# Optimization experiments

Measured on AMD Instinct MI355X. Metric: run time of the kernel, lower is better.

## Reference

```python
import jax, jax.numpy as jnp
import numpy as np

IMG = 160      # img_size
P = 100        # img_pathch_num = (160/16)^2
NBLK = 256     # pixels per 16x16 patch
NCLS = 4

def _index_matrix():
    # faithful port of NewAIFV.index_init
    ind = np.arange(256)
    start = (ind // 16) * IMG + (ind % 16) * 16
    idx = np.zeros(NBLK * P, dtype=np.int32)
    for i in range(P):
        idx[i * 256:(i + 1) * 256] = start + (i // 16) * 16 * IMG + (i % 16)
    return jnp.asarray(idx)

_IDX = _index_matrix()


def setup_inputs() -> dict:
    key = jax.random.key(0)
    ks = jax.random.split(key, 7)
    B, C = 4, 256
    return {
        "feat_S": jax.random.normal(ks[0], (B, C, IMG, IMG), jnp.float32),
        "feat_T": jax.random.normal(ks[1], (B, C, IMG, IMG), jnp.float32),
        "Pred_S": jax.random.normal(ks[2], (B, NCLS, IMG, IMG), jnp.float32),
        "Pred_T": jax.random.normal(ks[3], (B, NCLS, IMG, IMG), jnp.float32),
        "S_atten": jax.random.normal(ks[4], (B, P, P), jnp.float32),
        "T_atten": jax.random.normal(ks[5], (B, P, P), jnp.float32),
        "target": jax.random.randint(ks[6], (B, 1, IMG, IMG), 0, NCLS, jnp.int32),
    }


def _cos(a, b):
    # torch.nn.CosineSimilarity(dim=1): dot / max(|a||b|, 1e-8)
    num = (a * b).sum(1)
    den = jnp.maximum(jnp.sqrt((a * a).sum(1)) * jnp.sqrt((b * b).sum(1)), 1e-8)
    return num / den


def reference(feat_S, feat_T, Pred_S, Pred_T, S_atten, T_atten, target):
    B, C, H, W = feat_S.shape
    hw = H * W
    idx = _IDX
    # gathered patch reorder (index_select along flattened spatial dim)
    fS = feat_S.reshape(B, C, hw)[:, :, idx]
    fT = feat_T.reshape(B, C, hw)[:, :, idx]
    tg = target.reshape(B, 1, hw)[:, :, idx].reshape(B, 1, H, W)
    # 256-iteration loop of per-patch [B,C,100]@[B,100,100] matmuls -> one einsum
    TS = jnp.einsum('bcik,bkj->bcij', fS.reshape(B, C, NBLK, P), S_atten).reshape(B, C, H, W)
    TT = jnp.einsum('bcik,bkj->bcij', fT.reshape(B, C, NBLK, P), T_atten).reshape(B, C, H, W)
    ScS = jax.nn.softmax(Pred_S, axis=1).reshape(B, NCLS, hw)[:, :, idx].reshape(B, NCLS, H, W)
    ScT = jax.nn.softmax(Pred_T, axis=1).reshape(B, NCLS, hw)[:, :, idx].reshape(B, NCLS, H, W)
    dt = TS.dtype
    one_hot = (tg == jnp.arange(NCLS)[None, :, None, None]).astype(dt)   # [B,4,H,W]
    wei_s = (ScS * one_hot).sum(1)  # [B,H,W]
    wei_t = (ScT * one_hot).sum(1)
    tf = tg.astype(dt)  # [B,1,H,W], broadcast replaces nn.Upsample+expand

    def centers(class_list, s_prto, t_prto, eps):
        cS, cT = TS, TT
        for i in range(NCLS):
            j = class_list[i]
            stmp = ScT[:, j:j + 1]              # [B,1,H,W] (Score_Tmp, broadcast over C)
            m = (tf == i).astype(dt)            # mask_feat (class i)
            mp = (tf == j).astype(dt)           # mask_feat_prto (class class_list[i])
            denS = (mp if s_prto else m).sum((-1, -2)) + eps          # [B,1]
            protoS = ((mp * TS).sum((-1, -2)) / denS)[:, :, None, None]
            denT = (stmp * (mp if t_prto else m)).sum((-1, -2)) + eps
            protoT = ((mp * TT * stmp).sum((-1, -2)) / denT)[:, :, None, None]
            cS = (1 - m) * cS + m * protoS
            cT = (1 - m) * cT + m * protoT
        return cS, cT

    # three variants exactly as in the torch loops (denominator choices differ)
    cS0, cT0 = centers([1, 0, 3, 2], False, False, 1e-6)
    cS1, cT1 = centers([2, 3, 0, 1], True, True, 1e-6)
    cS2, cT2 = centers([3, 2, 1, 0], True, True, 1.0)

    w = (1 - wei_s) * wei_t
    vec_s = jnp.stack([w * _cos(TS, c) for c in (cS0, cS1, cS2)], axis=1)  # [B,3,H,W]
    vec_t = jnp.stack([w * _cos(TT, c) for c in (cT0, cT1, cT2)], axis=1)
    return jnp.mean((vec_s - vec_t) ** 2)
```

## Files before the change

kernel.cpp:

```cpp
#include <hip/hip_runtime.h>
#include <cstdint>
#include <cstddef>

#define HW 25600

typedef __attribute__((ext_vector_type(8))) short bf16x8;
typedef __attribute__((ext_vector_type(16))) float f32x16;

union ABu { bf16x8 v; uint2 u[2]; };
union B128 { bf16x8 v; int4 q; };

__device__ __forceinline__ f32x16 zero16() {
    f32x16 z;
#pragma unroll
    for (int i = 0; i < 16; ++i) z[i] = 0.f;
    return z;
}

__device__ __forceinline__ unsigned short f2bf(float x) {
    unsigned u = __builtin_bit_cast(unsigned, x);
    unsigned r = (u + 0x7FFF + ((u >> 16) & 1)) >> 16;
    return (unsigned short)r;
}

__device__ __forceinline__ float bf2f(unsigned short s) {
    return __builtin_bit_cast(float, (unsigned)s << 16);
}

__device__ __forceinline__ float wred(float v) {
#pragma unroll
    for (int off = 32; off; off >>= 1) v += __shfl_down(v, off, 64);
    return v;
}

__device__ double blockReduce256D(double v, double* s4) {
#pragma unroll
    for (int off = 32; off; off >>= 1) v += __shfl_down(v, off, 64);
    __syncthreads();
    if ((threadIdx.x & 63) == 0) s4[threadIdx.x >> 6] = v;
    __syncthreads();
    return s4[0] + s4[1] + s4[2] + s4[3];
}

__global__ __launch_bounds__(256) void k1_prep(
    const float* __restrict__ PredS, const float* __restrict__ PredT,
    const int* __restrict__ target,
    int* __restrict__ cls_arr, float* __restrict__ wT_arr,
    float* __restrict__ w_arr, float* __restrict__ partial_prep)
{
    __shared__ float sL[4][20];
    int blk = blockIdx.x;
    int b = blk / 100, r = blk - b * 100;
    int t = threadIdx.x, w = t >> 6, lane = t & 63;
    int ql = r * 256 + t;
    int v = ((t >> 4) * 160) + ((t & 15) * 16) + ((r >> 4) * 2560) + (r & 15);

    int cls = target[b * HW + v];

    const float* pS = PredS + b * 4 * HW + v;
    float a0 = pS[0], a1 = pS[HW], a2 = pS[2 * HW], a3 = pS[3 * HW];
    float mS = fmaxf(fmaxf(a0, a1), fmaxf(a2, a3));
    float e0 = expf(a0 - mS), e1 = expf(a1 - mS), e2 = expf(a2 - mS), e3 = expf(a3 - mS);
    float invS = 1.0f / (e0 + e1 + e2 + e3);
    float wei_s = ((cls == 0) ? e0 : (cls == 1) ? e1 : (cls == 2) ? e2 : e3) * invS;

    const float* pT = PredT + b * 4 * HW + v;
    float c0 = pT[0], c1 = pT[HW], c2 = pT[2 * HW], c3 = pT[3 * HW];
    float mT = fmaxf(fmaxf(c0, c1), fmaxf(c2, c3));
    float f0 = expf(c0 - mT), f1 = expf(c1 - mT), f2 = expf(c2 - mT), f3 = expf(c3 - mT);
    float invT = 1.0f / (f0 + f1 + f2 + f3);
    float tn0 = f0 * invT, tn1 = f1 * invT, tn2 = f2 * invT, tn3 = f3 * invT;
    float wei_t = (cls == 0) ? tn0 : (cls == 1) ? tn1 : (cls == 2) ? tn2 : tn3;

    cls_arr[b * HW + ql] = cls;
    wT_arr[b * HW + ql] = wei_t;
    w_arr[b * HW + ql] = (1.0f - wei_s) * wei_t;

    float vals[20];
#pragma unroll
    for (int s = 0; s < 4; ++s) vals[s] = (cls == s) ? 1.f : 0.f;
#pragma unroll
    for (int i2 = 0; i2 < 4; ++i2) {
        vals[4 + i2 * 4 + 0] = (cls == i2) ? tn0 : 0.f;
        vals[4 + i2 * 4 + 1] = (cls == i2) ? tn1 : 0.f;
        vals[4 + i2 * 4 + 2] = (cls == i2) ? tn2 : 0.f;
        vals[4 + i2 * 4 + 3] = (cls == i2) ? tn3 : 0.f;
    }
#pragma unroll
    for (int s = 0; s < 20; ++s) {
        float rv = wred(vals[s]);
        if (lane == 0) sL[w][s] = rv;
    }
    __syncthreads();
    if (t < 20) {
        int ob = blk * 20;
        partial_prep[ob + t] = sL[0][t] + sL[1][t] + sL[2][t] + sL[3][t];
    }
}

__global__ __launch_bounds__(128) void k2_w(
    const float* __restrict__ Satt, const float* __restrict__ Tatt,
    const int* __restrict__ cls_arr, const float* __restrict__ wT_arr,
    unsigned short* __restrict__ Wbf_S, unsigned short* __restrict__ Wbf_T,
    const float* __restrict__ partial_prep, float* __restrict__ cnt, float* __restrict__ E)
{
    int blk = blockIdx.x;
    int t = threadIdx.x;
    if (blk >= 1024) {
        int i = blk - 1024;
        if (t < 64) {
            int b = i / 20, s = i - (i / 20) * 20;
            float a = partial_prep[(b * 100 + t) * 20 + s];
            if (t + 64 < 100) a += partial_prep[(b * 100 + t + 64) * 20 + s];
            a = wred(a);
            if (t == 0) { if (s < 4) cnt[b * 4 + s] = a; else E[b * 16 + (s - 4)] = a; }
        }
        return;
    }
    __shared__ float Al[100 * 101];
    __shared__ int cls_s[100];
    __shared__ float wTs[100];
    int b = blk >> 8, i = blk & 255;
    if (t < 100) {
        cls_s[t] = cls_arr[b * HW + i * 100 + t];
        wTs[t] = wT_arr[b * HW + i * 100 + t];
    }
    for (int f = t; f < 10000; f += 128) Al[f + f / 100] = Satt[b * 10000 + f];
    __syncthreads();
    if (t < 100) {
        float a0 = 0, a1 = 0, a2 = 0, a3 = 0;
        for (int jc = 0; jc < 100; ++jc) {
            float a = Al[t * 101 + jc];
            int cc = cls_s[jc];
            a0 += (cc == 0) ? a : 0.f;
            a1 += (cc == 1) ? a : 0.f;
            a2 += (cc == 2) ? a : 0.f;
            a3 += (cc == 3) ? a : 0.f;
        }
        uint2 pk;
        pk.x = (unsigned)f2bf(a0) | ((unsigned)f2bf(a1) << 16);
        pk.y = (unsigned)f2bf(a2) | ((unsigned)f2bf(a3) << 16);
        *(uint2*)(Wbf_S + (size_t)(b * HW + i * 100 + t) * 4) = pk;
    }
    __syncthreads();
    for (int f = t; f < 10000; f += 128) Al[f + f / 100] = Tatt[b * 10000 + f];
    __syncthreads();
    if (t < 100) {
        float a0 = 0, a1 = 0, a2 = 0, a3 = 0;
        for (int jc = 0; jc < 100; ++jc) {
            float a = Al[t * 101 + jc] * wTs[jc];
            int cc = cls_s[jc];
            a0 += (cc == 0) ? a : 0.f;
            a1 += (cc == 1) ? a : 0.f;
            a2 += (cc == 2) ? a : 0.f;
            a3 += (cc == 3) ? a : 0.f;
        }
        uint2 pk;
        pk.x = (unsigned)f2bf(a0) | ((unsigned)f2bf(a1) << 16);
        pk.y = (unsigned)f2bf(a2) | ((unsigned)f2bf(a3) << 16);
        *(uint2*)(Wbf_T + (size_t)(b * HW + i * 100 + t) * 4) = pk;
    }
}

__global__ __launch_bounds__(256, 2) void k3_scan(
    const float* __restrict__ featS, const float* __restrict__ featT,
    const unsigned short* __restrict__ WbfS, const unsigned short* __restrict__ WbfT,
    unsigned short* __restrict__ featP, float* __restrict__ pp)
{
    __shared__ unsigned short ldsW[2][16 * 260 + 8];
    __shared__ float sL[16];
    int x = blockIdx.x;
    int side = x & 1;
    int rest = x >> 1;
    int cq = rest & 63;
    int bd = rest >> 6;
    int D = bd % 7, b = bd / 7;
    int t = threadIdx.x, w = t >> 6, lane = t & 63;

    const float* feat = side ? featT : featS;
    const unsigned short* Wbf = side ? WbfT : WbfS;
    unsigned short* fP = featP + (size_t)side * 26214400u;
    int ppbase = side * 28672 + ((b * 7 + D) * 256) * 4;

    int nr = (D < 6) ? 2 : 1;
    bool act = !(D == 6 && t >= 128);

    int4 w4[2][4];
#pragma unroll
    for (int rep = 0; rep < 2; ++rep) {
        if (rep < nr && act) {
            int Pb = D * 4096 + rep * 2048 + t * 8;
            const int4* wp = (const int4*)(Wbf + ((size_t)b * HW + Pb) * 4);
            w4[rep][0] = wp[0]; w4[rep][1] = wp[1]; w4[rep][2] = wp[2]; w4[rep][3] = wp[3];
        }
    }

    const float* fc0 = feat + (size_t)(b * 256 + cq * 4) * HW + 2560 * D;
    int lofs = 4 * (t & 63);

    float4 pf[4];
#pragma unroll
    for (int ra = 0; ra < 4; ++ra)
        pf[ra] = *(const float4*)(fc0 + 160 * ((t >> 6) + 4 * ra) + lofs);

    for (int cv = 0; cv < 4; ++cv) {
        unsigned short* lbuf = ldsW[cv & 1];
#pragma unroll
        for (int ra = 0; ra < 4; ++ra) {
            int A = (t >> 6) + 4 * ra;
            uint2 pk;
            pk.x = (unsigned)f2bf(pf[ra].x) | ((unsigned)f2bf(pf[ra].y) << 16);
            pk.y = (unsigned)f2bf(pf[ra].z) | ((unsigned)f2bf(pf[ra].w) << 16);
            *(uint2*)(lbuf + A * 260 + lofs) = pk;
        }
        __syncthreads();

        if (cv < 3) {
            const float* fcn = fc0 + (size_t)(cv + 1) * HW;
#pragma unroll
            for (int ra = 0; ra < 4; ++ra)
                pf[ra] = *(const float4*)(fcn + 160 * ((t >> 6) + 4 * ra) + lofs);
        }

        int c = cq * 4 + cv;
        float as0 = 0.f, as1 = 0.f, as2 = 0.f, as3 = 0.f;
        if (act) {
#pragma unroll
            for (int rep = 0; rep < 2; ++rep) {
                if (rep < nr) {
                    int Pb = D * 4096 + rep * 2048 + t * 8;
                    int A2 = (t & 31) >> 1;
                    int base_unit = A2 * 260 + 128 * (t & 1) + rep * 8 + (t >> 5);
                    unsigned short us[8];
                    float fv[8];
#pragma unroll
                    for (int e = 0; e < 8; ++e) {
                        us[e] = lbuf[base_unit + 16 * e];
                        fv[e] = bf2f(us[e]);
                    }
                    const unsigned short* ww = (const unsigned short*)w4[rep];
#pragma unroll
                    for (int e = 0; e < 8; ++e) {
                        as0 += fv[e] * bf2f(ww[e * 4 + 0]);
                        as1 += fv[e] * bf2f(ww[e * 4 + 1]);
                        as2 += fv[e] * bf2f(ww[e * 4 + 2]);
                        as3 += fv[e] * bf2f(ww[e * 4 + 3]);
                    }
                    int4 outp;
                    ((unsigned*)&outp)[0] = (unsigned)us[0] | ((unsigned)us[1] << 16);
                    ((unsigned*)&outp)[1] = (unsigned)us[2] | ((unsigned)us[3] << 16);
                    ((unsigned*)&outp)[2] = (unsigned)us[4] | ((unsigned)us[5] << 16);
                    ((unsigned*)&outp)[3] = (unsigned)us[6] | ((unsigned)us[7] << 16);
                    *(int4*)(fP + (size_t)(b * 256 + c) * HW + Pb) = outp;
                }
            }
        }

        float rv0 = wred(as0), rv1 = wred(as1), rv2 = wred(as2), rv3 = wred(as3);
        if (lane == 0) {
            sL[w * 4 + 0] = rv0; sL[w * 4 + 1] = rv1;
            sL[w * 4 + 2] = rv2; sL[w * 4 + 3] = rv3;
        }
        __syncthreads();
        if (t < 4) pp[ppbase + c * 4 + t] = sL[t] + sL[4 + t] + sL[8 + t] + sL[12 + t];
    }
}

__global__ __launch_bounds__(256, 2) void k4_mfma(
    const unsigned short* __restrict__ featP,
    const float* __restrict__ SattG, const float* __restrict__ TattG,
    const float* __restrict__ pp,
    float* __restrict__ n2S, float* __restrict__ n2T,
    float* __restrict__ dotS, float* __restrict__ dotT)
{
    __shared__ __align__(16) unsigned short featL[32 * 408 + 16];
    __shared__ __align__(16) unsigned short attL[100 * 136];
    __shared__ __align__(16) float SumL[128 * 4];

    int x = blockIdx.x;
    int side = x & 1, chalf = (x >> 1) & 1, b = (x >> 2) & 3, g = x >> 4;
    int t = threadIdx.x, w = t >> 6, l = t & 63;

    const float* Att = side ? TattG : SattG;
    const unsigned short* fP = featP + (size_t)side * 26214400u;
    float* n2h = side ? n2T : n2S;
    float* doth = side ? dotT : dotS;

    for (int f = t; f < 13600; f += 256) attL[f] = 0;
    featL[(t >> 3) * 408 + 400 + (t & 7)] = 0;
    if (t < 16) featL[32 * 408 + t] = 0;
    __syncthreads();
    for (int f = t; f < 10000; f += 256) {
        int k = f / 100, j = f - k * 100;
        attL[j * 136 + k] = f2bf(Att[b * 10000 + f]);
    }
#pragma unroll
    for (int f0 = 0; f0 < 2; ++f0) {
        int f = f0 * 256 + t;
        int cl = f >> 2, j = f & 3;
        float s = 0.f;
#pragma unroll
        for (int D = 0; D < 7; ++D)
            s += pp[side * 28672 + ((b * 7 + D) * 256 + chalf * 128 + cl) * 4 + j];
        SumL[f] = s;
    }
    __syncthreads();

    int lj = l & 31, lh = l >> 5;
    bf16x8 breg[7][4];
    {
        int j3 = 96 + lj; if (j3 > 99) j3 = 99;
        int rowoff[4] = { lj, 32 + lj, 64 + lj, j3 };
#pragma unroll
        for (int ks = 0; ks < 7; ++ks)
#pragma unroll
            for (int s = 0; s < 4; ++s)
                breg[ks][s] = ((const B128*)(attL + rowoff[s] * 136 + lh * 8 + ks * 16))->v;
    }

    float n2a[4] = {0, 0, 0, 0};
    float dota[4][4] = {};
    const unsigned short* arow = featL + lj * 408 + w * 100 + lh * 8;

#pragma unroll 1
    for (int ch = 0; ch < 4; ++ch) {
        __syncthreads();
        {
            const unsigned short* src = fP + (size_t)(b * 256 + chalf * 128 + ch * 32 + (t >> 3)) * HW
                                        + g * 400 + (t & 7) * 8;
            unsigned short* dst = featL + (t >> 3) * 408 + (t & 7) * 8;
#pragma unroll
            for (int i = 0; i < 7; ++i) {
                int cb = (t & 7) + i * 8;
                if (cb < 50)
                    *(int4*)(dst + i * 64) = *(const int4*)(src + i * 64);
            }
        }
        __syncthreads();

        f32x16 acc0 = zero16(), acc1 = zero16(), acc2 = zero16(), acc3 = zero16();
#pragma unroll
        for (int ks = 0; ks < 7; ++ks) {
            ABu aF;
            aF.u[0] = *(const uint2*)(arow + ks * 16);
            aF.u[1] = *(const uint2*)(arow + ks * 16 + 4);
            acc0 = __builtin_amdgcn_mfma_f32_32x32x16_bf16(aF.v, breg[ks][0], acc0, 0, 0, 0);
            acc1 = __builtin_amdgcn_mfma_f32_32x32x16_bf16(aF.v, breg[ks][1], acc1, 0, 0, 0);
            acc2 = __builtin_amdgcn_mfma_f32_32x32x16_bf16(aF.v, breg[ks][2], acc2, 0, 0, 0);
            acc3 = __builtin_amdgcn_mfma_f32_32x32x16_bf16(aF.v, breg[ks][3], acc3, 0, 0, 0);
        }

        int cb0 = ch * 32 + (lh << 2);
#pragma unroll
        for (int r = 0; r < 16; ++r) {
            int cl = (r & 3) + ((r >> 2) << 3);
            float4 sv = *(const float4*)(SumL + (size_t)(cb0 + cl) * 4);
            float v;
            v = acc0[r]; n2a[0] += v * v;
            dota[0][0] += v * sv.x; dota[0][1] += v * sv.y; dota[0][2] += v * sv.z; dota[0][3] += v * sv.w;
            v = acc1[r]; n2a[1] += v * v;
            dota[1][0] += v * sv.x; dota[1][1] += v * sv.y; dota[1][2] += v * sv.z; dota[1][3] += v * sv.w;
            v = acc2[r]; n2a[2] += v * v;
            dota[2][0] += v * sv.x; dota[2][1] += v * sv.y; dota[2][2] += v * sv.z; dota[2][3] += v * sv.w;
            v = acc3[r]; n2a[3] += v * v;
            dota[3][0] += v * sv.x; dota[3][1] += v * sv.y; dota[3][2] += v * sv.z; dota[3][3] += v * sv.w;
        }
    }

#pragma unroll
    for (int nt = 0; nt < 4; ++nt) {
        n2a[nt] += __shfl_down(n2a[nt], 32, 64);
#pragma unroll
        for (int m = 0; m < 4; ++m) dota[nt][m] += __shfl_down(dota[nt][m], 32, 64);
    }
    if (l < 32) {
        int i0 = g * 4 + w;
        int pqb = b * HW + i0 * 100;
#pragma unroll
        for (int nt = 0; nt < 4; ++nt) {
            int j = nt * 32 + l;
            if (j < 100) {
                n2h[chalf * 102400 + pqb + j] = n2a[nt];
                float4 dv = {dota[nt][0], dota[nt][1], dota[nt][2], dota[nt][3]};
                *(float4*)(doth + chalf * 409600 + (size_t)(pqb + j) * 4) = dv;
            }
        }
    }
}

__global__ void k45_tbl(const float* __restrict__ pp,
                        const float* __restrict__ cnt, const float* __restrict__ E,
                        float* __restrict__ tbl)
{
    int blk = blockIdx.x, t = threadIdx.x;
    if (blk < 32) {
        int b = blk >> 3, sj = blk & 7, stv = sj >> 2, j = sj & 3;
        float s = 0.f;
#pragma unroll
        for (int u = 0; u < 4; ++u) {
            int c = t * 4 + u;
            float xx = 0.f;
#pragma unroll
            for (int D = 0; D < 7; ++D)
                xx += pp[stv * 28672 + ((b * 7 + D) * 256 + c) * 4 + j];
            s += xx * xx;
        }
        s = wred(s);
        if (t == 0) tbl[b * 32 + stv * 4 + j] = sqrtf(s);
    } else if (t < 16) {
        int b = t >> 2, i = t & 3;
        tbl[b * 32 + 8 + 0 * 4 + i] = cnt[b * 4 + i] + 1e-6f;
        tbl[b * 32 + 8 + 1 * 4 + i] = cnt[b * 4 + (i ^ 2)] + 1e-6f;
        tbl[b * 32 + 8 + 2 * 4 + i] = cnt[b * 4 + (i ^ 3)] + 1.0f;
        tbl[b * 32 + 20 + 0 * 4 + i] = E[b * 16 + i * 4 + (i ^ 1)] + 1e-6f;
        tbl[b * 32 + 20 + 1 * 4 + i] = E[b * 16 + 5 * (i ^ 2)] + 1e-6f;
        tbl[b * 32 + 20 + 2 * 4 + i] = E[b * 16 + 5 * (i ^ 3)] + 1.0f;
    }
}

__global__ __launch_bounds__(256) void k5_final(
    const int* __restrict__ cls_arr, const float* __restrict__ w_arr,
    const float* __restrict__ n2S, const float* __restrict__ n2T,
    const float* __restrict__ dotS, const float* __restrict__ dotT,
    const float* __restrict__ tbl, double* __restrict__ partial_res)
{
    __shared__ double s4[4];
    int blk = blockIdx.x;
    int b = blk / 100, r = blk - b * 100;
    int t = threadIdx.x;
    int pq = b * HW + r * 256 + t;

    int i = cls_arr[pq];
    float wv = w_arr[pq];
    float sqS = sqrtf(n2S[pq] + n2S[102400 + pq]);
    float sqT = sqrtf(n2T[pq] + n2T[102400 + pq]);
    float4 dSa = *(const float4*)(dotS + (size_t)pq * 4);
    float4 dSb = *(const float4*)(dotS + 409600 + (size_t)pq * 4);
    float4 dTa = *(const float4*)(dotT + (size_t)pq * 4);
    float4 dTb = *(const float4*)(dotT + 409600 + (size_t)pq * 4);
    float4 dS = {dSa.x + dSb.x, dSa.y + dSb.y, dSa.z + dSb.z, dSa.w + dSb.w};
    float4 dT = {dTa.x + dTb.x, dTa.y + dTb.y, dTa.z + dTb.z, dTa.w + dTb.w};
    const float* tb = tbl + b * 32;

    double acc = 0.0;
#pragma unroll
    for (int v = 0; v < 3; ++v) {
        int j = i ^ (v + 1);
        float dsj = (j == 0) ? dS.x : (j == 1) ? dS.y : (j == 2) ? dS.z : dS.w;
        float dtj = (j == 0) ? dT.x : (j == 1) ? dT.y : (j == 2) ? dT.z : dT.w;
        float cnS = tb[j], cnT = tb[4 + j];
        float denS = tb[8 + v * 4 + i], denT = tb[20 + v * 4 + i];
        float cs = (dsj / denS) / fmaxf(sqS * (cnS / denS), 1e-8f);
        float ct = (dtj / denT) / fmaxf(sqT * (cnT / denT), 1e-8f);
        float vs = wv * cs, vt = wv * ct;
        float d = vs - vt;
        acc += (double)d * (double)d;
    }
    double tot = blockReduce256D(acc, s4);
    if (t == 0) partial_res[blk] = tot;
}

__global__ __launch_bounds__(256) void k6_out(const double* __restrict__ partial_res,
                                              float* __restrict__ out)
{
    __shared__ double s4[4];
    int t = threadIdx.x;
    double v = (t < 200) ? (partial_res[t] + partial_res[t + 200]) : 0.0;
    double tot = blockReduce256D(v, s4);
    if (t == 0) out[0] = (float)(tot / 307200.0);
}

extern "C" void kernel_launch(void* const* d_in, const int* in_sizes, int n_in,
                              void* d_out, int out_size, void* d_ws, size_t ws_size,
                              hipStream_t stream)
{
    const float* feat_S  = (const float*)d_in[0];
    const float* feat_T  = (const float*)d_in[1];
    const float* Pred_S  = (const float*)d_in[2];
    const float* Pred_T  = (const float*)d_in[3];
    const float* S_atten = (const float*)d_in[4];
    const float* T_atten = (const float*)d_in[5];
    const int*   target  = (const int*)d_in[6];

    float* ws = (float*)d_ws;
    unsigned short* featP = (unsigned short*)d_ws;
    unsigned short* WbfS  = (unsigned short*)(ws + 26214400);
    unsigned short* WbfT  = (unsigned short*)(ws + 26419200);
    int*   cls_a = (int*)(ws + 26624000);
    float* wT_a  = ws + 26726400;
    float* w_a   = ws + 26828800;
    float* n2S   = ws + 26939392;
    float* n2T   = ws + 27144192;
    float* dotS  = ws + 27348992;
    float* dotT  = ws + 28168192;
    float* pprep = ws + 28987392;
    float* cnt   = ws + 28995392;
    float* E     = ws + 28995408;
    float* tbl   = ws + 28995472;
    double* pres = (double*)(ws + 28995600);
    float* ppart = ws + 28996400;

    k1_prep<<<400, 256, 0, stream>>>(Pred_S, Pred_T, target, cls_a, wT_a, w_a, pprep);
    k2_w<<<1104, 128, 0, stream>>>(S_atten, T_atten, cls_a, wT_a, WbfS, WbfT, pprep, cnt, E);
    k3_scan<<<3584, 256, 0, stream>>>(feat_S, feat_T, WbfS, WbfT, featP, ppart);
    k4_mfma<<<1024, 256, 0, stream>>>(featP, S_atten, T_atten, ppart, n2S, n2T, dotS, dotT);
    k45_tbl<<<33, 64, 0, stream>>>(ppart, cnt, E, tbl);
    k5_final<<<400, 256, 0, stream>>>(cls_a, w_a, n2S, n2T, dotS, dotT, tbl, pres);
    k6_out<<<1, 256, 0, stream>>>(pres, (float*)d_out);
}
```

Baseline: 146.1 us.

## Fuse table build and final reduction into k5 with last-block atomic

Removes the separate k45_tbl and k6_out kernels. Each k5 block recomputes its batch's norm and denominator table in shared memory, and the last block to finish (tracked by an atomic counter) performs the final reduction. This cuts two kernel launches and the dependency gaps between them. In exchange it adds redundant per-block table recomputation, a memset of the counter, and extra barriers.

```diff
diff --git a/kernel.cpp b/kernel.cpp
--- a/kernel.cpp
+++ b/kernel.cpp
@@ -388,48 +388,56 @@
     }
 }
 
-__global__ void k45_tbl(const float* __restrict__ pp,
-                        const float* __restrict__ cnt, const float* __restrict__ E,
-                        float* __restrict__ tbl)
-{
-    int blk = blockIdx.x, t = threadIdx.x;
-    if (blk < 32) {
-        int b = blk >> 3, sj = blk & 7, stv = sj >> 2, j = sj & 3;
-        float s = 0.f;
-#pragma unroll
-        for (int u = 0; u < 4; ++u) {
-            int c = t * 4 + u;
-            float xx = 0.f;
-#pragma unroll
-            for (int D = 0; D < 7; ++D)
-                xx += pp[stv * 28672 + ((b * 7 + D) * 256 + c) * 4 + j];
-            s += xx * xx;
-        }
-        s = wred(s);
-        if (t == 0) tbl[b * 32 + stv * 4 + j] = sqrtf(s);
-    } else if (t < 16) {
-        int b = t >> 2, i = t & 3;
-        tbl[b * 32 + 8 + 0 * 4 + i] = cnt[b * 4 + i] + 1e-6f;
-        tbl[b * 32 + 8 + 1 * 4 + i] = cnt[b * 4 + (i ^ 2)] + 1e-6f;
-        tbl[b * 32 + 8 + 2 * 4 + i] = cnt[b * 4 + (i ^ 3)] + 1.0f;
-        tbl[b * 32 + 20 + 0 * 4 + i] = E[b * 16 + i * 4 + (i ^ 1)] + 1e-6f;
-        tbl[b * 32 + 20 + 1 * 4 + i] = E[b * 16 + 5 * (i ^ 2)] + 1e-6f;
-        tbl[b * 32 + 20 + 2 * 4 + i] = E[b * 16 + 5 * (i ^ 3)] + 1.0f;
-    }
-}
-
 __global__ __launch_bounds__(256) void k5_final(
     const int* __restrict__ cls_arr, const float* __restrict__ w_arr,
     const float* __restrict__ n2S, const float* __restrict__ n2T,
     const float* __restrict__ dotS, const float* __restrict__ dotT,
-    const float* __restrict__ tbl, double* __restrict__ partial_res)
+    const float* __restrict__ pp, const float* __restrict__ cnt,
+    const float* __restrict__ E,
+    double* __restrict__ partial_res, unsigned* __restrict__ counter,
+    float* __restrict__ out)
 {
+    __shared__ float tbl_s[32];
+    __shared__ float sf[4];
     __shared__ double s4[4];
+    __shared__ int lastflag;
     int blk = blockIdx.x;
     int b = blk / 100, r = blk - b * 100;
     int t = threadIdx.x;
+
+    float xx[8];
+    {
+        int c = t;
+#pragma unroll
+        for (int s = 0; s < 8; ++s) {
+            int stv = s >> 2, j = s & 3;
+            float a = 0.f;
+#pragma unroll
+            for (int D = 0; D < 7; ++D)
+                a += pp[stv * 28672 + ((b * 7 + D) * 256 + c) * 4 + j];
+            xx[s] = a * a;
+        }
+    }
+#pragma unroll
+    for (int s = 0; s < 8; ++s) {
+        float rv = wred(xx[s]);
+        __syncthreads();
+        if ((t & 63) == 0) sf[t >> 6] = rv;
+        __syncthreads();
+        if (t == 0) tbl_s[s] = sqrtf(sf[0] + sf[1] + sf[2] + sf[3]);
+    }
+    if (t < 4) {
+        int i = t;
+        tbl_s[8 + 0 * 4 + i]  = cnt[b * 4 + i] + 1e-6f;
+        tbl_s[8 + 1 * 4 + i]  = cnt[b * 4 + (i ^ 2)] + 1e-6f;
+        tbl_s[8 + 2 * 4 + i]  = cnt[b * 4 + (i ^ 3)] + 1.0f;
+        tbl_s[20 + 0 * 4 + i] = E[b * 16 + i * 4 + (i ^ 1)] + 1e-6f;
+        tbl_s[20 + 1 * 4 + i] = E[b * 16 + 5 * (i ^ 2)] + 1e-6f;
+        tbl_s[20 + 2 * 4 + i] = E[b * 16 + 5 * (i ^ 3)] + 1.0f;
+    }
+    __syncthreads();
+
     int pq = b * HW + r * 256 + t;
-
     int i = cls_arr[pq];
     float wv = w_arr[pq];
     float sqS = sqrtf(n2S[pq] + n2S[102400 + pq]);
@@ -440,7 +448,7 @@
     float4 dTb = *(const float4*)(dotT + 409600 + (size_t)pq * 4);
     float4 dS = {dSa.x + dSb.x, dSa.y + dSb.y, dSa.z + dSb.z, dSa.w + dSb.w};
     float4 dT = {dTa.x + dTb.x, dTa.y + dTb.y, dTa.z + dTb.z, dTa.w + dTb.w};
-    const float* tb = tbl + b * 32;
+    const float* tb = tbl_s;
 
     double acc = 0.0;
 #pragma unroll
@@ -457,17 +465,19 @@
         acc += (double)d * (double)d;
     }
     double tot = blockReduce256D(acc, s4);
-    if (t == 0) partial_res[blk] = tot;
-}
-
-__global__ __launch_bounds__(256) void k6_out(const double* __restrict__ partial_res,
-                                              float* __restrict__ out)
-{
-    __shared__ double s4[4];
-    int t = threadIdx.x;
-    double v = (t < 200) ? (partial_res[t] + partial_res[t + 200]) : 0.0;
-    double tot = blockReduce256D(v, s4);
-    if (t == 0) out[0] = (float)(tot / 307200.0);
+    if (t == 0) {
+        partial_res[blk] = tot;
+        __threadfence();
+        unsigned rank = atomicAdd(counter, 1u);
+        lastflag = (rank == 399u) ? 1 : 0;
+    }
+    __syncthreads();
+    if (lastflag) {
+        __threadfence();
+        double v = (t < 200) ? (partial_res[t] + partial_res[t + 200]) : 0.0;
+        double tt = blockReduce256D(v, s4);
+        if (t == 0) out[0] = (float)(tt / 307200.0);
+    }
 }
 
 extern "C" void kernel_launch(void* const* d_in, const int* in_sizes, int n_in,
@@ -496,15 +506,15 @@
     float* pprep = ws + 28987392;
     float* cnt   = ws + 28995392;
     float* E     = ws + 28995408;
-    float* tbl   = ws + 28995472;
+    unsigned* counter = (unsigned*)(ws + 28995472);
     double* pres = (double*)(ws + 28995600);
     float* ppart = ws + 28996400;
 
+    hipMemsetAsync((void*)counter, 0, 4, stream);
     k1_prep<<<400, 256, 0, stream>>>(Pred_S, Pred_T, target, cls_a, wT_a, w_a, pprep);
     k2_w<<<1104, 128, 0, stream>>>(S_atten, T_atten, cls_a, wT_a, WbfS, WbfT, pprep, cnt, E);
     k3_scan<<<3584, 256, 0, stream>>>(feat_S, feat_T, WbfS, WbfT, featP, ppart);
     k4_mfma<<<1024, 256, 0, stream>>>(featP, S_atten, T_atten, ppart, n2S, n2T, dotS, dotT);
-    k45_tbl<<<33, 64, 0, stream>>>(ppart, cnt, E, tbl);
-    k5_final<<<400, 256, 0, stream>>>(cls_a, w_a, n2S, n2T, dotS, dotT, tbl, pres);
-    k6_out<<<1, 256, 0, stream>>>(pres, (float*)d_out);
-}
+    k5_final<<<400, 256, 0, stream>>>(cls_a, w_a, n2S, n2T, dotS, dotT,
+                                      ppart, cnt, E, pres, counter, (float*)d_out);
+}
```

New measurement: 158.8 us. +8.7%, slower.
